# Kernel optimization log

Hardware: AMD Instinct MI355X
Metric: run time of the kernel (lower is better)

The kernel has to match this reference:

```python
import jax, jax.numpy as jnp
import numpy as np

N_NODES = 50000
N_EDGES = 800000


def _sage(x, src, dst, Wl, Wr, b, n):
    # PyG SAGEConv: lin_l(mean aggr of neighbors) + lin_r(x) (+ bias in lin_l)
    agg = jax.ops.segment_sum(x[src], dst, num_segments=n)
    cnt = jax.ops.segment_sum(jnp.ones((src.shape[0],), x.dtype), dst, num_segments=n)
    mean = agg / jnp.maximum(cnt, 1.0)[:, None]
    return mean @ Wl + x @ Wr + b


def _gat(x, src, dst, W, att_src, att_dst, b, n):
    H, C = att_src.shape
    h = (x @ W).reshape(n, H, C)                      # [N,H,C]
    a_s = jnp.sum(h * att_src, axis=-1)               # [N,H]
    a_d = jnp.sum(h * att_dst, axis=-1)               # [N,H]
    e = jax.nn.leaky_relu(a_s[src] + a_d[dst], 0.2)   # [E,H]
    m = jax.ops.segment_max(e, dst, num_segments=n)   # per-dst softmax (stable)
    ex = jnp.exp(e - m[dst])
    s = jax.ops.segment_sum(ex, dst, num_segments=n)
    alpha = ex / (s[dst] + 1e-16)                     # [E,H]
    out = jax.ops.segment_sum(h[src] * alpha[:, :, None], dst, num_segments=n)
    return out.reshape(n, H * C) + b


def setup_inputs() -> dict:
    key = jax.random.key(0)
    ks = jax.random.split(key, 16)
    F_IN, H1, GH, HEADS, H2, NC = 20, 256, 32, 4, 256, 5
    GOUT = GH * HEADS
    sc = 0.05
    return {
        "x": jax.random.normal(ks[0], (N_NODES, F_IN), jnp.float32),
        "edge_index": jax.random.randint(ks[1], (2, N_EDGES), 0, N_NODES, jnp.int32),
        "sage1_Wl": jax.random.normal(ks[2], (F_IN, H1), jnp.float32) * sc,
        "sage1_Wr": jax.random.normal(ks[3], (F_IN, H1), jnp.float32) * sc,
        "sage1_b": jnp.zeros((H1,), jnp.float32),
        "gat_W": jax.random.normal(ks[4], (H1, GOUT), jnp.float32) * sc,
        "gat_att_src": jax.random.normal(ks[5], (HEADS, GH), jnp.float32) * sc,
        "gat_att_dst": jax.random.normal(ks[6], (HEADS, GH), jnp.float32) * sc,
        "gat_b": jnp.zeros((GOUT,), jnp.float32),
        "sage2_Wl": jax.random.normal(ks[7], (GOUT, H2), jnp.float32) * sc,
        "sage2_Wr": jax.random.normal(ks[8], (GOUT, H2), jnp.float32) * sc,
        "sage2_b": jnp.zeros((H2,), jnp.float32),
        "cls_W": jax.random.normal(ks[9], (H2, NC), jnp.float32) * sc,
        "cls_b": jnp.zeros((NC,), jnp.float32),
    }


def reference(x, edge_index, sage1_Wl, sage1_Wr, sage1_b, gat_W, gat_att_src,
              gat_att_dst, gat_b, sage2_Wl, sage2_Wr, sage2_b, cls_W, cls_b):
    n = x.shape[0]
    src, dst = edge_index[0], edge_index[1]
    h = jax.nn.relu(_sage(x, src, dst, sage1_Wl, sage1_Wr, sage1_b, n))
    h = jax.nn.elu(_gat(h, src, dst, gat_W, gat_att_src, gat_att_dst, gat_b, n))
    h = jax.nn.relu(_sage(h, src, dst, sage2_Wl, sage2_Wr, sage2_b, n))
    return h @ cls_W + cls_b
```

## Files before the change

### kernel.cpp

```cpp
#include <hip/hip_runtime.h>
#include <math.h>

#define N_NODES 50000
#define N_EDGES 800000
#define TPB 256
#define NCHUNK ((N_NODES + 255) / 256)

typedef short s16x8 __attribute__((ext_vector_type(8)));
typedef float f32x4 __attribute__((ext_vector_type(4)));

__device__ __forceinline__ unsigned short f2bf(float f) {
    unsigned u = __float_as_uint(f);
    u += 0x7fffu + ((u >> 16) & 1u);
    return (unsigned short)(u >> 16);
}
__device__ __forceinline__ float bf2f(unsigned short h) {
    return __uint_as_float(((unsigned)h) << 16);
}

__global__ void wt_all_k(const float* __restrict__ s1Wl, const float* __restrict__ s1Wr,
                         const float* __restrict__ gW, const float* __restrict__ s2Wl,
                         const float* __restrict__ s2Wr, unsigned short* __restrict__ Wt1,
                         unsigned short* __restrict__ Wt2, unsigned short* __restrict__ Wt3,
                         int* __restrict__ deg) {
    int idx = blockIdx.x * TPB + threadIdx.x;
    if (idx < N_NODES) deg[idx] = 0;
    if (idx < 16384) {
        int n = idx >> 6, k = idx & 63;
        float v = 0.f;
        if (k < 20) v = s1Wl[k * 256 + n];
        else if (k < 40) v = s1Wr[(k - 20) * 256 + n];
        Wt1[idx] = f2bf(v);
    } else if (idx < 49152) {
        int j = idx - 16384;
        int n = j >> 8, k = j & 255;
        Wt2[j] = f2bf(gW[(size_t)k * 128 + n]);
    } else if (idx < 114688) {
        int j = idx - 49152;
        int n = j >> 8, k = j & 255;
        float v = (k < 128) ? s2Wl[(size_t)k * 256 + n] : s2Wr[(size_t)(k - 128) * 256 + n];
        Wt3[j] = f2bf(v);
    }
}

template<int ACT>
__global__ void gemm_mfma(const float* __restrict__ A1, int K1,
                          const float* __restrict__ A2, int K2,
                          const unsigned short* __restrict__ Wt, int Kp,
                          const float* __restrict__ bias,
                          unsigned short* __restrict__ outb, int NO) {
    constexpr int BM = 128, BK = 32, LDP = 40;
    __shared__ unsigned short sA[BM * LDP];
    __shared__ unsigned short sB[128 * LDP];
    const int K = K1 + K2;
    const int T = Kp / BK;
    const int tid = threadIdx.x;
    const int lane = tid & 63, wid = tid >> 6;
    const int wr = wid >> 1, wc = wid & 1;
    const int row0 = blockIdx.y * BM, col0 = blockIdx.x * 128;
    const int l15 = lane & 15, l4 = lane >> 4;
    f32x4 acc[4][4] = {};

    for (int t = 0; t < T; ++t) {
        __syncthreads();
#pragma unroll
        for (int j = 0; j < 4; ++j) {
            int e = tid + j * 256;
            int r = e >> 3, k4 = e & 7;
            int kg = t * BK + k4 * 4, mg = row0 + r;
            float4 v = {0.f, 0.f, 0.f, 0.f};
            if (mg < N_NODES) {
                if (kg < K1)     v = *(const float4*)&A1[(size_t)mg * K1 + kg];
                else if (kg < K) v = *(const float4*)&A2[(size_t)mg * K2 + (kg - K1)];
            }
            ushort4 b;
            b.x = f2bf(v.x); b.y = f2bf(v.y); b.z = f2bf(v.z); b.w = f2bf(v.w);
            *(ushort4*)&sA[r * LDP + k4 * 4] = b;
        }
#pragma unroll
        for (int j = 0; j < 2; ++j) {
            int e = tid + j * 256;
            int n = e >> 2, k8 = e & 3;
            int4 v = *(const int4*)&Wt[(size_t)(col0 + n) * Kp + t * BK + k8 * 8];
            *(int4*)&sB[n * LDP + k8 * 8] = v;
        }
        __syncthreads();
        s16x8 af[4], bfr[4];
#pragma unroll
        for (int i = 0; i < 4; ++i) {
            af[i]  = *(const s16x8*)&sA[(wr * 64 + i * 16 + l15) * LDP + l4 * 8];
            bfr[i] = *(const s16x8*)&sB[(wc * 64 + i * 16 + l15) * LDP + l4 * 8];
        }
#pragma unroll
        for (int mi = 0; mi < 4; ++mi)
#pragma unroll
            for (int ni = 0; ni < 4; ++ni)
                acc[mi][ni] = __builtin_amdgcn_mfma_f32_16x16x32_bf16(
                    af[mi], bfr[ni], acc[mi][ni], 0, 0, 0);
    }
#pragma unroll
    for (int mi = 0; mi < 4; ++mi) {
#pragma unroll
        for (int ni = 0; ni < 4; ++ni) {
            int col = col0 + wc * 64 + ni * 16 + l15;
            float bb = bias ? bias[col] : 0.f;
#pragma unroll
            for (int r = 0; r < 4; ++r) {
                int row = row0 + wr * 64 + mi * 16 + l4 * 4 + r;
                if (row < N_NODES) {
                    float v = acc[mi][ni][r] + bb;
                    if (ACT) v = fmaxf(v, 0.f);
                    outb[(size_t)row * NO + col] = f2bf(v);
                }
            }
        }
    }
}

template<int ACT, int CLS>
__global__ void gemm_mfma_bf(const unsigned short* __restrict__ A1, int K1,
                             const unsigned short* __restrict__ A2, int K2,
                             const unsigned short* __restrict__ Wt, int Kp,
                             const float* __restrict__ bias,
                             unsigned short* __restrict__ outb, int NO,
                             const float* __restrict__ clsW, float* __restrict__ pp) {
    constexpr int BM = 128, BK = 32, LDP = 40;
    __shared__ unsigned short sA[BM * LDP];
    __shared__ unsigned short sB[128 * LDP];
    const int T = Kp / BK;
    const int tid = threadIdx.x;
    const int lane = tid & 63, wid = tid >> 6;
    const int wr = wid >> 1, wc = wid & 1;
    const int row0 = blockIdx.y * BM, col0 = blockIdx.x * 128;
    const int l15 = lane & 15, l4 = lane >> 4;
    f32x4 acc[4][4] = {};

    for (int t = 0; t < T; ++t) {
        __syncthreads();
#pragma unroll
        for (int j = 0; j < 2; ++j) {
            int e = tid + j * 256;
            int r = e >> 2, k8 = e & 3;
            int kg = t * BK + k8 * 8, mg = row0 + r;
            int4 v = {0, 0, 0, 0};
            if (mg < N_NODES) {
                if (kg < K1) v = *(const int4*)&A1[(size_t)mg * K1 + kg];
                else         v = *(const int4*)&A2[(size_t)mg * K2 + (kg - K1)];
            }
            *(int4*)&sA[r * LDP + k8 * 8] = v;
        }
#pragma unroll
        for (int j = 0; j < 2; ++j) {
            int e = tid + j * 256;
            int n = e >> 2, k8 = e & 3;
            int4 v = *(const int4*)&Wt[(size_t)(col0 + n) * Kp + t * BK + k8 * 8];
            *(int4*)&sB[n * LDP + k8 * 8] = v;
        }
        __syncthreads();
        s16x8 af[4], bfr[4];
#pragma unroll
        for (int i = 0; i < 4; ++i) {
            af[i]  = *(const s16x8*)&sA[(wr * 64 + i * 16 + l15) * LDP + l4 * 8];
            bfr[i] = *(const s16x8*)&sB[(wc * 64 + i * 16 + l15) * LDP + l4 * 8];
        }
#pragma unroll
        for (int mi = 0; mi < 4; ++mi)
#pragma unroll
            for (int ni = 0; ni < 4; ++ni)
                acc[mi][ni] = __builtin_amdgcn_mfma_f32_16x16x32_bf16(
                    af[mi], bfr[ni], acc[mi][ni], 0, 0, 0);
    }

    if (CLS == 0) {
#pragma unroll
        for (int mi = 0; mi < 4; ++mi) {
#pragma unroll
            for (int ni = 0; ni < 4; ++ni) {
                int col = col0 + wc * 64 + ni * 16 + l15;
                float bb = bias ? bias[col] : 0.f;
#pragma unroll
                for (int r = 0; r < 4; ++r) {
                    int row = row0 + wr * 64 + mi * 16 + l4 * 4 + r;
                    if (row < N_NODES) {
                        float v = acc[mi][ni][r] + bb;
                        if (ACT) v = fmaxf(v, 0.f);
                        outb[(size_t)row * NO + col] = f2bf(v);
                    }
                }
            }
        }
    } else {
        __syncthreads();
        float* sClsW = (float*)sA;
        float* cp    = (float*)sB;
        for (int i = tid; i < 640; i += 256)
            sClsW[i] = clsW[(size_t)(col0 + i / 5) * 5 + (i % 5)];
        __syncthreads();
        float bcol[4];
#pragma unroll
        for (int ni = 0; ni < 4; ++ni)
            bcol[ni] = bias[col0 + wc * 64 + ni * 16 + l15];
#pragma unroll
        for (int mi = 0; mi < 4; ++mi) {
#pragma unroll
            for (int r = 0; r < 4; ++r) {
                float p0 = 0.f, p1 = 0.f, p2 = 0.f, p3 = 0.f, p4 = 0.f;
#pragma unroll
                for (int ni = 0; ni < 4; ++ni) {
                    float v = fmaxf(acc[mi][ni][r] + bcol[ni], 0.f);
                    const float* w = &sClsW[(wc * 64 + ni * 16 + l15) * 5];
                    p0 = fmaf(v, w[0], p0); p1 = fmaf(v, w[1], p1);
                    p2 = fmaf(v, w[2], p2); p3 = fmaf(v, w[3], p3);
                    p4 = fmaf(v, w[4], p4);
                }
#pragma unroll
                for (int msk = 1; msk < 16; msk <<= 1) {
                    p0 += __shfl_xor(p0, msk, 16);
                    p1 += __shfl_xor(p1, msk, 16);
                    p2 += __shfl_xor(p2, msk, 16);
                    p3 += __shfl_xor(p3, msk, 16);
                    p4 += __shfl_xor(p4, msk, 16);
                }
                if (l15 == 0) {
                    int rr = wr * 64 + mi * 16 + l4 * 4 + r;
                    float* d = &cp[(wc * 128 + rr) * 5];
                    d[0] = p0; d[1] = p1; d[2] = p2; d[3] = p3; d[4] = p4;
                }
            }
        }
        __syncthreads();
        for (int i = tid; i < 640; i += 256) {
            int rr = i / 5, cc = i - rr * 5;
            int row = row0 + rr;
            if (row < N_NODES)
                pp[(size_t)blockIdx.x * ((size_t)N_NODES * 5) + (size_t)row * 5 + cc]
                    = cp[rr * 5 + cc] + cp[(128 + rr) * 5 + cc];
        }
    }
}

__global__ void combine_k(const float* __restrict__ pp, const float* __restrict__ clsb,
                          float* __restrict__ out) {
    int idx = blockIdx.x * TPB + threadIdx.x;
    if (idx >= N_NODES * 5) return;
    int c = idx % 5;
    out[idx] = pp[idx] + pp[(size_t)N_NODES * 5 + idx] + clsb[c];
}

__global__ void hist_k(const int* __restrict__ dst, int* __restrict__ deg) {
    int e = blockIdx.x * TPB + threadIdx.x;
    if (e < N_EDGES) atomicAdd(&deg[dst[e]], 1);
}

__global__ void scan1_k(const int* __restrict__ deg, int* __restrict__ rowptr,
                        int* __restrict__ bsum) {
    __shared__ int tmp[256];
    int tid = threadIdx.x;
    int idx = blockIdx.x * 256 + tid;
    int v = (idx < N_NODES) ? deg[idx] : 0;
    tmp[tid] = v;
    __syncthreads();
    for (int off = 1; off < 256; off <<= 1) {
        int t = (tid >= off) ? tmp[tid - off] : 0;
        __syncthreads();
        tmp[tid] += t;
        __syncthreads();
    }
    if (idx < N_NODES) rowptr[idx] = tmp[tid] - v;
    if (tid == 255) bsum[blockIdx.x] = tmp[255];
}

__global__ void scan2_k(int* __restrict__ bsum) {
    __shared__ int tmp[256];
    int tid = threadIdx.x;
    int v = (tid < NCHUNK) ? bsum[tid] : 0;
    tmp[tid] = v;
    __syncthreads();
    for (int off = 1; off < 256; off <<= 1) {
        int t = (tid >= off) ? tmp[tid - off] : 0;
        __syncthreads();
        tmp[tid] += t;
        __syncthreads();
    }
    if (tid < NCHUNK) bsum[tid] = tmp[tid] - v;
}

__global__ void scan3_k(int* __restrict__ rowptr, const int* __restrict__ bsum) {
    int idx = blockIdx.x * 256 + threadIdx.x;
    if (idx < N_NODES) rowptr[idx] += bsum[blockIdx.x];
    if (idx == 0) rowptr[N_NODES] = N_EDGES;
}

__global__ void fill_k(const int* __restrict__ src, const int* __restrict__ dst,
                       const int* __restrict__ rowptr, int* __restrict__ deg,
                       int* __restrict__ csr_src) {
    int e = blockIdx.x * TPB + threadIdx.x;
    if (e >= N_EDGES) return;
    int d = dst[e];
    int r = atomicSub(&deg[d], 1) - 1;
    csr_src[rowptr[d] + r] = src[e];
}

__global__ void gm20_k(const int* __restrict__ rowptr, const int* __restrict__ csr_src,
                       const float* __restrict__ feat, float* __restrict__ out) {
    int tid = threadIdx.x;
    int n = blockIdx.x * 8 + (tid >> 5);
    int c = tid & 31;
    if (n >= N_NODES || c >= 20) return;
    int e0 = rowptr[n], e1 = rowptr[n + 1];
    float acc = 0.f;
    int e = e0;
    for (; e + 1 < e1; e += 2) {
        acc += feat[(size_t)csr_src[e] * 20 + c] + feat[(size_t)csr_src[e + 1] * 20 + c];
    }
    if (e < e1) acc += feat[(size_t)csr_src[e] * 20 + c];
    out[(size_t)n * 20 + c] = acc / fmaxf((float)(e1 - e0), 1.0f);
}

__global__ void gather_mean_bf(const int* __restrict__ rowptr, const int* __restrict__ csr_src,
                               const unsigned short* __restrict__ featb,
                               unsigned short* __restrict__ outb) {
    int tid = threadIdx.x;
    int n = blockIdx.x * 8 + (tid >> 5);
    int c = tid & 31;
    int e0 = rowptr[n], e1 = rowptr[n + 1];
    float4 acc = {0.f, 0.f, 0.f, 0.f};
    int e = e0;
    for (; e + 7 < e1; e += 8) {
        ushort4 u[8];
#pragma unroll
        for (int j = 0; j < 8; ++j)
            u[j] = *(const ushort4*)&featb[(size_t)csr_src[e + j] * 128 + c * 4];
#pragma unroll
        for (int j = 0; j < 8; ++j) {
            acc.x += bf2f(u[j].x); acc.y += bf2f(u[j].y);
            acc.z += bf2f(u[j].z); acc.w += bf2f(u[j].w);
        }
    }
    for (; e < e1; ++e) {
        ushort4 u = *(const ushort4*)&featb[(size_t)csr_src[e] * 128 + c * 4];
        acc.x += bf2f(u.x); acc.y += bf2f(u.y); acc.z += bf2f(u.z); acc.w += bf2f(u.w);
    }
    float inv = 1.0f / fmaxf((float)(e1 - e0), 1.0f);
    ushort4 o;
    o.x = f2bf(acc.x * inv); o.y = f2bf(acc.y * inv);
    o.z = f2bf(acc.z * inv); o.w = f2bf(acc.w * inv);
    *(ushort4*)&outb[(size_t)n * 128 + c * 4] = o;
}

__global__ void att_scores_bf(const unsigned short* __restrict__ hb,
                              const float* __restrict__ att_src,
                              const float* __restrict__ att_dst,
                              float* __restrict__ as_, float* __restrict__ ad_) {
    int idx = blockIdx.x * TPB + threadIdx.x;
    if (idx >= N_NODES * 4) return;
    int n = idx >> 2, hd = idx & 3;
    const unsigned short* row = hb + (size_t)n * 128 + hd * 32;
    float sa = 0.f, sd = 0.f;
#pragma unroll
    for (int c4 = 0; c4 < 8; ++c4) {
        ushort4 u = *(const ushort4*)&row[c4 * 4];
        const float* asr = &att_src[hd * 32 + c4 * 4];
        const float* adr = &att_dst[hd * 32 + c4 * 4];
        sa = fmaf(bf2f(u.x), asr[0], sa); sd = fmaf(bf2f(u.x), adr[0], sd);
        sa = fmaf(bf2f(u.y), asr[1], sa); sd = fmaf(bf2f(u.y), adr[1], sd);
        sa = fmaf(bf2f(u.z), asr[2], sa); sd = fmaf(bf2f(u.z), adr[2], sd);
        sa = fmaf(bf2f(u.w), asr[3], sa); sd = fmaf(bf2f(u.w), adr[3], sd);
    }
    as_[idx] = sa;
    ad_[idx] = sd;
}

__global__ void gat_gather_bf(const int* __restrict__ rowptr, const int* __restrict__ csr_src,
                              const unsigned short* __restrict__ hb,
                              const float* __restrict__ as_, const float* __restrict__ ad_,
                              const float* __restrict__ gb,
                              unsigned short* __restrict__ outb) {
    int tid = threadIdx.x;
    int n = blockIdx.x * 8 + (tid >> 5);
    int c = tid & 31;
    int hd = c >> 3;
    int q = c & 7;
    int e0 = rowptr[n], e1 = rowptr[n + 1];
    float ad = ad_[n * 4 + hd];
    float m = -INFINITY, s = 0.f;
    float4 acc = {0.f, 0.f, 0.f, 0.f};
    int e = e0;
    for (; e + 7 < e1; e += 8) {
        int sq = csr_src[e + q];
        float aq = as_[sq * 4 + hd] + ad;
        aq = aq >= 0.f ? aq : 0.2f * aq;
        float pm = aq;
        pm = fmaxf(pm, __shfl_xor(pm, 1, 8));
        pm = fmaxf(pm, __shfl_xor(pm, 2, 8));
        pm = fmaxf(pm, __shfl_xor(pm, 4, 8));
        if (pm > m) {
            float sc = __expf(m - pm);
            s *= sc; acc.x *= sc; acc.y *= sc; acc.z *= sc; acc.w *= sc;
            m = pm;
        }
        float exq = __expf(aq - m);
        float exs[8];
        int   sj[8];
#pragma unroll
        for (int j = 0; j < 8; ++j) {
            exs[j] = __shfl(exq, j, 8);
            sj[j]  = __shfl(sq, j, 8);
        }
        s += ((exs[0] + exs[1]) + (exs[2] + exs[3]))
           + ((exs[4] + exs[5]) + (exs[6] + exs[7]));
        ushort4 u[8];
#pragma unroll
        for (int j = 0; j < 8; ++j)
            u[j] = *(const ushort4*)&hb[(size_t)sj[j] * 128 + c * 4];
#pragma unroll
        for (int j = 0; j < 8; ++j) {
            float ex = exs[j];
            acc.x = fmaf(bf2f(u[j].x), ex, acc.x);
            acc.y = fmaf(bf2f(u[j].y), ex, acc.y);
            acc.z = fmaf(bf2f(u[j].z), ex, acc.z);
            acc.w = fmaf(bf2f(u[j].w), ex, acc.w);
        }
    }
    for (; e < e1; ++e) {
        int s0 = csr_src[e];
        float a = as_[s0 * 4 + hd] + ad;
        a = a >= 0.f ? a : 0.2f * a;
        if (a > m) {
            float sc = __expf(m - a);
            s *= sc; acc.x *= sc; acc.y *= sc; acc.z *= sc; acc.w *= sc;
            m = a;
        }
        float ex = __expf(a - m);
        s += ex;
        ushort4 u = *(const ushort4*)&hb[(size_t)s0 * 128 + c * 4];
        acc.x = fmaf(bf2f(u.x), ex, acc.x); acc.y = fmaf(bf2f(u.y), ex, acc.y);
        acc.z = fmaf(bf2f(u.z), ex, acc.z); acc.w = fmaf(bf2f(u.w), ex, acc.w);
    }
    float inv = 1.0f / (s + 1e-16f);
    float rx = acc.x * inv + gb[c * 4 + 0];
    float ry = acc.y * inv + gb[c * 4 + 1];
    float rz = acc.z * inv + gb[c * 4 + 2];
    float rw = acc.w * inv + gb[c * 4 + 3];
    rx = rx > 0.f ? rx : expm1f(rx);
    ry = ry > 0.f ? ry : expm1f(ry);
    rz = rz > 0.f ? rz : expm1f(rz);
    rw = rw > 0.f ? rw : expm1f(rw);
    ushort4 o;
    o.x = f2bf(rx); o.y = f2bf(ry); o.z = f2bf(rz); o.w = f2bf(rw);
    *(ushort4*)&outb[(size_t)n * 128 + c * 4] = o;
}

extern "C" void kernel_launch(void* const* d_in, const int* in_sizes, int n_in,
                              void* d_out, int out_size, void* d_ws, size_t ws_size,
                              hipStream_t stream) {
    const float* x    = (const float*)d_in[0];
    const int*   ei   = (const int*)d_in[1];
    const float* s1Wl = (const float*)d_in[2];
    const float* s1Wr = (const float*)d_in[3];
    const float* s1b  = (const float*)d_in[4];
    const float* gW   = (const float*)d_in[5];
    const float* gas  = (const float*)d_in[6];
    const float* gad  = (const float*)d_in[7];
    const float* gb   = (const float*)d_in[8];
    const float* s2Wl = (const float*)d_in[9];
    const float* s2Wr = (const float*)d_in[10];
    const float* s2b  = (const float*)d_in[11];
    const float* clsW = (const float*)d_in[12];
    const float* clsb = (const float*)d_in[13];
    float* out = (float*)d_out;
    const int* src = ei;
    const int* dst = ei + N_EDGES;

    float* ws  = (float*)d_ws;
    float* M20  = ws;
    float* as_  = M20 + (size_t)N_NODES * 20;
    float* ad_  = as_ + N_NODES * 4;
    float* pp   = ad_ + N_NODES * 4;
    int* deg     = (int*)(pp + (size_t)2 * N_NODES * 5);
    int* bsum    = deg + N_NODES;
    int* rowptr  = bsum + 256;
    int* csr_src = rowptr + N_NODES + 4;
    unsigned short* Wt1 = (unsigned short*)(csr_src + N_EDGES);
    unsigned short* Wt2 = Wt1 + 256 * 64;
    unsigned short* Wt3 = Wt2 + 128 * 256;
    unsigned short* Ab  = Wt3 + 256 * 256;
    unsigned short* Cb  = Ab + (size_t)N_NODES * 256;
    unsigned short* Db  = Cb + (size_t)N_NODES * 128;
    unsigned short* Mb  = Db + (size_t)N_NODES * 128;

    const int MB = (N_NODES + 127) / 128;

    wt_all_k<<<(114688 + TPB - 1) / TPB, TPB, 0, stream>>>(s1Wl, s1Wr, gW, s2Wl, s2Wr,
                                                           Wt1, Wt2, Wt3, deg);

    hist_k<<<(N_EDGES + TPB - 1) / TPB, TPB, 0, stream>>>(dst, deg);
    scan1_k<<<NCHUNK, 256, 0, stream>>>(deg, rowptr, bsum);
    scan2_k<<<1, 256, 0, stream>>>(bsum);
    scan3_k<<<NCHUNK, 256, 0, stream>>>(rowptr, bsum);
    fill_k<<<(N_EDGES + TPB - 1) / TPB, TPB, 0, stream>>>(src, dst, rowptr, deg, csr_src);

    gm20_k<<<(N_NODES + 7) / 8, 256, 0, stream>>>(rowptr, csr_src, x, M20);
    gemm_mfma<1><<<dim3(2, MB), 256, 0, stream>>>(M20, 20, x, 20, Wt1, 64, s1b, Ab, 256);

    gemm_mfma_bf<0, 0><<<dim3(1, MB), 256, 0, stream>>>(Ab, 256, nullptr, 0, Wt2, 256,
                                                        nullptr, Cb, 128, nullptr, nullptr);
    att_scores_bf<<<(N_NODES * 4 + TPB - 1) / TPB, TPB, 0, stream>>>(Cb, gas, gad, as_, ad_);
    gat_gather_bf<<<N_NODES / 8, 256, 0, stream>>>(rowptr, csr_src, Cb, as_, ad_, gb, Db);

    gather_mean_bf<<<N_NODES / 8, 256, 0, stream>>>(rowptr, csr_src, Db, Mb);
    gemm_mfma_bf<1, 1><<<dim3(2, MB), 256, 0, stream>>>(Mb, 128, Db, 128, Wt3, 256, s2b,
                                                        nullptr, 256, clsW, pp);

    combine_k<<<(N_NODES * 5 + TPB - 1) / TPB, TPB, 0, stream>>>(pp, clsb, out);
}
```

Baseline: 299.2 us.

## Fuse GAT attention scores into projection GEMM epilogue; simplify gather loop

```diff
diff --git a/kernel.cpp b/kernel.cpp
--- a/kernel.cpp
+++ b/kernel.cpp
@@ -117,13 +117,16 @@
     }
 }
 
-template<int ACT, int CLS>
+template<int ACT, int CLS, int ATT>
 __global__ void gemm_mfma_bf(const unsigned short* __restrict__ A1, int K1,
                              const unsigned short* __restrict__ A2, int K2,
                              const unsigned short* __restrict__ Wt, int Kp,
                              const float* __restrict__ bias,
                              unsigned short* __restrict__ outb, int NO,
-                             const float* __restrict__ clsW, float* __restrict__ pp) {
+                             const float* __restrict__ clsW, float* __restrict__ pp,
+                             const float* __restrict__ att_src,
+                             const float* __restrict__ att_dst,
+                             float* __restrict__ as_, float* __restrict__ ad_) {
     constexpr int BM = 128, BK = 32, LDP = 40;
     __shared__ unsigned short sA[BM * LDP];
     __shared__ unsigned short sB[128 * LDP];
@@ -171,7 +174,45 @@
                     af[mi], bfr[ni], acc[mi][ni], 0, 0, 0);
     }
 
-    if (CLS == 0) {
+    if (ATT) {
+        float atts[4], attd[4];
+#pragma unroll
+        for (int ni = 0; ni < 4; ++ni) {
+            int ai = (wc * 2 + (ni >> 1)) * 32 + (ni & 1) * 16 + l15;
+            atts[ni] = att_src[ai];
+            attd[ni] = att_dst[ai];
+        }
+#pragma unroll
+        for (int mi = 0; mi < 4; ++mi) {
+#pragma unroll
+            for (int r = 0; r < 4; ++r) {
+                int row = row0 + wr * 64 + mi * 16 + l4 * 4 + r;
+                float sa0 = 0.f, sd0 = 0.f, sa1 = 0.f, sd1 = 0.f;
+#pragma unroll
+                for (int ni = 0; ni < 4; ++ni) {
+                    int col = wc * 64 + ni * 16 + l15;
+                    unsigned short hb = f2bf(acc[mi][ni][r]);
+                    if (row < N_NODES) outb[(size_t)row * 128 + col] = hb;
+                    float v = bf2f(hb);
+                    if (ni < 2) { sa0 = fmaf(v, atts[ni], sa0); sd0 = fmaf(v, attd[ni], sd0); }
+                    else        { sa1 = fmaf(v, atts[ni], sa1); sd1 = fmaf(v, attd[ni], sd1); }
+                }
+#pragma unroll
+                for (int msk = 1; msk < 16; msk <<= 1) {
+                    sa0 += __shfl_xor(sa0, msk, 16);
+                    sd0 += __shfl_xor(sd0, msk, 16);
+                    sa1 += __shfl_xor(sa1, msk, 16);
+                    sd1 += __shfl_xor(sd1, msk, 16);
+                }
+                if (l15 == 0 && row < N_NODES) {
+                    as_[row * 4 + wc * 2]     = sa0;
+                    ad_[row * 4 + wc * 2]     = sd0;
+                    as_[row * 4 + wc * 2 + 1] = sa1;
+                    ad_[row * 4 + wc * 2 + 1] = sd1;
+                }
+            }
+        }
+    } else if (CLS == 0) {
 #pragma unroll
         for (int mi = 0; mi < 4; ++mi) {
 #pragma unroll
@@ -348,29 +389,6 @@
     *(ushort4*)&outb[(size_t)n * 128 + c * 4] = o;
 }
 
-__global__ void att_scores_bf(const unsigned short* __restrict__ hb,
-                              const float* __restrict__ att_src,
-                              const float* __restrict__ att_dst,
-                              float* __restrict__ as_, float* __restrict__ ad_) {
-    int idx = blockIdx.x * TPB + threadIdx.x;
-    if (idx >= N_NODES * 4) return;
-    int n = idx >> 2, hd = idx & 3;
-    const unsigned short* row = hb + (size_t)n * 128 + hd * 32;
-    float sa = 0.f, sd = 0.f;
-#pragma unroll
-    for (int c4 = 0; c4 < 8; ++c4) {
-        ushort4 u = *(const ushort4*)&row[c4 * 4];
-        const float* asr = &att_src[hd * 32 + c4 * 4];
-        const float* adr = &att_dst[hd * 32 + c4 * 4];
-        sa = fmaf(bf2f(u.x), asr[0], sa); sd = fmaf(bf2f(u.x), adr[0], sd);
-        sa = fmaf(bf2f(u.y), asr[1], sa); sd = fmaf(bf2f(u.y), adr[1], sd);
-        sa = fmaf(bf2f(u.z), asr[2], sa); sd = fmaf(bf2f(u.z), adr[2], sd);
-        sa = fmaf(bf2f(u.w), asr[3], sa); sd = fmaf(bf2f(u.w), adr[3], sd);
-    }
-    as_[idx] = sa;
-    ad_[idx] = sd;
-}
-
 __global__ void gat_gather_bf(const int* __restrict__ rowptr, const int* __restrict__ csr_src,
                               const unsigned short* __restrict__ hb,
                               const float* __restrict__ as_, const float* __restrict__ ad_,
@@ -380,47 +398,42 @@
     int n = blockIdx.x * 8 + (tid >> 5);
     int c = tid & 31;
     int hd = c >> 3;
-    int q = c & 7;
     int e0 = rowptr[n], e1 = rowptr[n + 1];
     float ad = ad_[n * 4 + hd];
     float m = -INFINITY, s = 0.f;
     float4 acc = {0.f, 0.f, 0.f, 0.f};
     int e = e0;
-    for (; e + 7 < e1; e += 8) {
-        int sq = csr_src[e + q];
-        float aq = as_[sq * 4 + hd] + ad;
-        aq = aq >= 0.f ? aq : 0.2f * aq;
-        float pm = aq;
-        pm = fmaxf(pm, __shfl_xor(pm, 1, 8));
-        pm = fmaxf(pm, __shfl_xor(pm, 2, 8));
-        pm = fmaxf(pm, __shfl_xor(pm, 4, 8));
+    for (; e + 3 < e1; e += 4) {
+        int s0 = csr_src[e], s1 = csr_src[e + 1], s2 = csr_src[e + 2], s3 = csr_src[e + 3];
+        float a0 = as_[s0 * 4 + hd] + ad;
+        float a1 = as_[s1 * 4 + hd] + ad;
+        float a2 = as_[s2 * 4 + hd] + ad;
+        float a3 = as_[s3 * 4 + hd] + ad;
+        a0 = a0 >= 0.f ? a0 : 0.2f * a0;
+        a1 = a1 >= 0.f ? a1 : 0.2f * a1;
+        a2 = a2 >= 0.f ? a2 : 0.2f * a2;
+        a3 = a3 >= 0.f ? a3 : 0.2f * a3;
+        float pm = fmaxf(fmaxf(a0, a1), fmaxf(a2, a3));
         if (pm > m) {
             float sc = __expf(m - pm);
             s *= sc; acc.x *= sc; acc.y *= sc; acc.z *= sc; acc.w *= sc;
             m = pm;
         }
-        float exq = __expf(aq - m);
-        float exs[8];
-        int   sj[8];
-#pragma unroll
-        for (int j = 0; j < 8; ++j) {
-            exs[j] = __shfl(exq, j, 8);
-            sj[j]  = __shfl(sq, j, 8);
-        }
-        s += ((exs[0] + exs[1]) + (exs[2] + exs[3]))
-           + ((exs[4] + exs[5]) + (exs[6] + exs[7]));
-        ushort4 u[8];
-#pragma unroll
-        for (int j = 0; j < 8; ++j)
-            u[j] = *(const ushort4*)&hb[(size_t)sj[j] * 128 + c * 4];
-#pragma unroll
-        for (int j = 0; j < 8; ++j) {
-            float ex = exs[j];
-            acc.x = fmaf(bf2f(u[j].x), ex, acc.x);
-            acc.y = fmaf(bf2f(u[j].y), ex, acc.y);
-            acc.z = fmaf(bf2f(u[j].z), ex, acc.z);
-            acc.w = fmaf(bf2f(u[j].w), ex, acc.w);
-        }
+        float ex0 = __expf(a0 - m), ex1 = __expf(a1 - m);
+        float ex2 = __expf(a2 - m), ex3 = __expf(a3 - m);
+        s += (ex0 + ex1) + (ex2 + ex3);
+        ushort4 u0 = *(const ushort4*)&hb[(size_t)s0 * 128 + c * 4];
+        ushort4 u1 = *(const ushort4*)&hb[(size_t)s1 * 128 + c * 4];
+        ushort4 u2 = *(const ushort4*)&hb[(size_t)s2 * 128 + c * 4];
+        ushort4 u3 = *(const ushort4*)&hb[(size_t)s3 * 128 + c * 4];
+        acc.x = fmaf(bf2f(u0.x), ex0, acc.x); acc.y = fmaf(bf2f(u0.y), ex0, acc.y);
+        acc.z = fmaf(bf2f(u0.z), ex0, acc.z); acc.w = fmaf(bf2f(u0.w), ex0, acc.w);
+        acc.x = fmaf(bf2f(u1.x), ex1, acc.x); acc.y = fmaf(bf2f(u1.y), ex1, acc.y);
+        acc.z = fmaf(bf2f(u1.z), ex1, acc.z); acc.w = fmaf(bf2f(u1.w), ex1, acc.w);
+        acc.x = fmaf(bf2f(u2.x), ex2, acc.x); acc.y = fmaf(bf2f(u2.y), ex2, acc.y);
+        acc.z = fmaf(bf2f(u2.z), ex2, acc.z); acc.w = fmaf(bf2f(u2.w), ex2, acc.w);
+        acc.x = fmaf(bf2f(u3.x), ex3, acc.x); acc.y = fmaf(bf2f(u3.y), ex3, acc.y);
+        acc.z = fmaf(bf2f(u3.z), ex3, acc.z); acc.w = fmaf(bf2f(u3.w), ex3, acc.w);
     }
     for (; e < e1; ++e) {
         int s0 = csr_src[e];
@@ -503,14 +516,15 @@
     gm20_k<<<(N_NODES + 7) / 8, 256, 0, stream>>>(rowptr, csr_src, x, M20);
     gemm_mfma<1><<<dim3(2, MB), 256, 0, stream>>>(M20, 20, x, 20, Wt1, 64, s1b, Ab, 256);
 
-    gemm_mfma_bf<0, 0><<<dim3(1, MB), 256, 0, stream>>>(Ab, 256, nullptr, 0, Wt2, 256,
-                                                        nullptr, Cb, 128, nullptr, nullptr);
-    att_scores_bf<<<(N_NODES * 4 + TPB - 1) / TPB, TPB, 0, stream>>>(Cb, gas, gad, as_, ad_);
+    gemm_mfma_bf<0, 0, 1><<<dim3(1, MB), 256, 0, stream>>>(
+        Ab, 256, nullptr, 0, Wt2, 256, nullptr, Cb, 128,
+        nullptr, nullptr, gas, gad, as_, ad_);
     gat_gather_bf<<<N_NODES / 8, 256, 0, stream>>>(rowptr, csr_src, Cb, as_, ad_, gb, Db);
 
     gather_mean_bf<<<N_NODES / 8, 256, 0, stream>>>(rowptr, csr_src, Db, Mb);
-    gemm_mfma_bf<1, 1><<<dim3(2, MB), 256, 0, stream>>>(Mb, 128, Db, 128, Wt3, 256, s2b,
-                                                        nullptr, 256, clsW, pp);
+    gemm_mfma_bf<1, 1, 0><<<dim3(2, MB), 256, 0, stream>>>(
+        Mb, 128, Db, 128, Wt3, 256, s2b, nullptr, 256, clsW, pp,
+        nullptr, nullptr, nullptr, nullptr);
 
     combine_k<<<(N_NODES * 5 + TPB - 1) / TPB, TPB, 0, stream>>>(pp, clsb, out);
 }
```

Result: faster. 286.9 us (-4.1%).
